# Optimization experiments

Hardware: AMD Instinct MI355X
Metric: run time of the kernel (lower is better)

The kernel has to match this reference:

```python
import jax, jax.numpy as jnp
import numpy as np

A = -0.75  # PyTorch bicubic convolution constant

def _cubic_weights(t):
    # t: fractional part in [0,1). Returns the 4 tap weights
    # (matches PyTorch get_cubic_upsample_coefficients with A=-0.75).
    t1 = t + 1.0
    w0 = ((A * t1 - 5.0 * A) * t1 + 8.0 * A) * t1 - 4.0 * A
    w1 = ((A + 2.0) * t - (A + 3.0)) * t * t + 1.0
    s = 1.0 - t
    w2 = ((A + 2.0) * s - (A + 3.0)) * s * s + 1.0
    s2 = 2.0 - t
    w3 = ((A * s2 - 5.0 * A) * s2 + 8.0 * A) * s2 - 4.0 * A
    return (w0, w1, w2, w3)

def _reflect_index(i, size):
    # integer reflection for padding_mode='reflection', align_corners=True over [0, size-1]
    span = size - 1
    if span <= 0:
        return jnp.zeros_like(i)
    m = jnp.abs(i) % (2 * span)
    return jnp.where(m > span, 2 * span - m, m)

def _bicubic_warp(x, flow):
    # x: [B,C,H,W], flow: [B,2,H,W] (flow[:,0]=dx, flow[:,1]=dy)
    B, C, H, W = x.shape
    gx = jnp.arange(W, dtype=x.dtype)
    gy = jnp.arange(H, dtype=x.dtype)
    # normalize-to-[-1,1] then grid_sample unnormalize (align_corners=True) cancel exactly:
    ix = gx[None, None, :] + flow[:, 0]  # [B,H,W] source x coord
    iy = gy[None, :, None] + flow[:, 1]  # [B,H,W] source y coord
    bx = jnp.floor(ix)
    by = jnp.floor(iy)
    tx = ix - bx
    ty = iy - by
    bx = bx.astype(jnp.int32)
    by = by.astype(jnp.int32)
    wx = _cubic_weights(tx)
    wy = _cubic_weights(ty)
    xf = x.reshape(B, C, H * W)
    out = jnp.zeros_like(x)
    for j in range(4):  # fixed 4x4 tap stencil
        Y = _reflect_index(by + (j - 1), H)
        for i in range(4):
            X = _reflect_index(bx + (i - 1), W)
            idx = (Y * W + X).reshape(B, 1, H * W)
            v = jnp.take_along_axis(xf, idx, axis=2).reshape(B, C, H, W)
            out = out + v * (wy[j] * wx[i])[:, None]
    return out

def setup_inputs() -> dict:
    key = jax.random.key(0)
    k1, k2, k3 = jax.random.split(key, 3)
    B, C, H, W = 8, 4, 1024, 1024
    return {
        "input": jax.random.normal(k1, (B, C, H, W), dtype=jnp.float32),
        "target": jax.random.normal(k2, (B, C, H, W), dtype=jnp.float32),
        "flow": jax.random.normal(k3, (B, 2, H, W), dtype=jnp.float32),
    }

def reference(input, target, flow):
    warped = _bicubic_warp(target, flow)
    b = 5
    return jnp.mean(jnp.abs(input[..., b:-b, b:-b] - warped[..., b:-b, b:-b]))
```

## Files before the change

kernel.cpp:

```cpp
#include <hip/hip_runtime.h>

constexpr int BB = 8, CC = 4, HH = 1024, WW = 1024, CROP = 5;
constexpr int HC = HH - 2 * CROP, WC = WW - 2 * CROP;
constexpr int HW = HH * WW;
constexpr float AA = -0.75f;

constexpr int NSTRIP = 16;
constexpr int GRID = 32 * NSTRIP * 2;
constexpr int RING = 16;
constexpr int SWID = 272;
constexpr int CH_STRIDE = RING * SWID;

typedef __attribute__((address_space(1))) const void gv_t;
typedef __attribute__((address_space(3))) void lv_t;

__device__ __forceinline__ int reflect_small(int i) {
    int r = i < 0 ? -i : i;
    return r > (HH - 1) ? 2 * (HH - 1) - r : r;
}

__device__ __forceinline__ void cubic_w(float t, float& w0, float& w1,
                                        float& w2, float& w3) {
    float t1 = t + 1.0f;
    w0 = ((AA * t1 - 5.0f * AA) * t1 + 8.0f * AA) * t1 - 4.0f * AA;
    w1 = ((AA + 2.0f) * t - (AA + 3.0f)) * t * t + 1.0f;
    float s = 1.0f - t;
    w2 = ((AA + 2.0f) * s - (AA + 3.0f)) * s * s + 1.0f;
    float s2 = 2.0f - t;
    w3 = ((AA * s2 - 5.0f * AA) * s2 + 8.0f * AA) * s2 - 4.0f * AA;
}

__device__ __noinline__ float px_slow2(const float* __restrict__ tgt_p,
                                       const float* __restrict__ in_p, int pix,
                                       int bx, int by, float wx0, float wx1,
                                       float wx2, float wx3, float wy0,
                                       float wy1, float wy2, float wy3) {
    const int r0 = reflect_small(by - 1) * WW;
    const int r1 = reflect_small(by) * WW;
    const int r2 = reflect_small(by + 1) * WW;
    const int r3 = reflect_small(by + 2) * WW;
    const int c0 = reflect_small(bx - 1);
    const int c1 = reflect_small(bx);
    const int c2 = reflect_small(bx + 1);
    const int c3 = reflect_small(bx + 2);
    float acc = 0.0f;
#pragma unroll
    for (int c = 0; c < 2; ++c) {
        const float* tb = tgt_p + c * HW;
        float q0 = wx0 * tb[r0 + c0] + wx1 * tb[r0 + c1] + wx2 * tb[r0 + c2] +
                   wx3 * tb[r0 + c3];
        float q1 = wx0 * tb[r1 + c0] + wx1 * tb[r1 + c1] + wx2 * tb[r1 + c2] +
                   wx3 * tb[r1 + c3];
        float q2 = wx0 * tb[r2 + c0] + wx1 * tb[r2 + c1] + wx2 * tb[r2 + c2] +
                   wx3 * tb[r2 + c3];
        float q3 = wx0 * tb[r3 + c0] + wx1 * tb[r3 + c1] + wx2 * tb[r3 + c2] +
                   wx3 * tb[r3 + c3];
        float v = wy0 * q0 + wy1 * q1 + wy2 * q2 + wy3 * q3;
        acc += fabsf(in_p[c * HW + pix] - v);
    }
    return acc;
}

__global__ __launch_bounds__(256, 4) void warp_loss_k(
    const float* __restrict__ input, const float* __restrict__ target,
    const float* __restrict__ flow, float* __restrict__ wsbuf) {
    __shared__ float cache[2 * CH_STRIDE];
    const int tid = (int)threadIdx.x;
    const int wv = tid >> 6, lane = tid & 63;

    const int low = (int)blockIdx.x & 511;
    const int pair = (int)blockIdx.x >> 9;
    const int colid = low >> 4;
    const int strip = low & 15;
    const int b = colid >> 2;
    const int chunk = colid & 3;
    const int x0 = CROP + chunk * 256;
    const int wscol = chunk == 0 ? 0 : chunk == 1 ? 252 : chunk == 2 ? 508 : 752;
    const int y0 = CROP + strip * 64;
    const int y1 = min(y0 + 64, CROP + HC);

    const int x = x0 + tid;
    const bool valid_px = x <= 1018;
    const int xc = valid_px ? x : 1018;

    const float* tgt_p = target + (size_t)b * CC * HW + (size_t)(pair * 2) * HW;
    const float* in_p = input + (size_t)b * CC * HW + (size_t)(pair * 2) * HW;
    const float* flow_b = flow + (size_t)b * 2 * HW;

    const int chv = wv >> 1, part = wv & 1;
    const float* plane = tgt_p + (size_t)chv * HW;
    const int chbase = chv * CH_STRIDE;

#pragma unroll 1
    for (int k = 0; k < 11; ++k) {
        const int r = y0 - 5 + k;
        const int slot = r & (RING - 1);
        const float* src = plane + (size_t)r * WW + wscol;
        if (part == 0) {
            __builtin_amdgcn_global_load_lds(
                (gv_t*)(src + lane * 4), (lv_t*)&cache[chbase + slot * SWID],
                16, 0, 0);
        } else {
            __builtin_amdgcn_global_load_lds(
                (gv_t*)(src + 208 + lane),
                (lv_t*)&cache[chbase + slot * SWID + 208], 4, 0, 0);
        }
    }
    __syncthreads();

    float lsum = 0.0f;

    for (int y = y0; y < y1; ++y) {
        {
            const int r = y + 6;
            if (r < HH) {
                const int slot = r & (RING - 1);
                const float* src = plane + (size_t)r * WW + wscol;
                if (part == 0) {
                    __builtin_amdgcn_global_load_lds(
                        (gv_t*)(src + lane * 4),
                        (lv_t*)&cache[chbase + slot * SWID], 16, 0, 0);
                } else {
                    __builtin_amdgcn_global_load_lds(
                        (gv_t*)(src + 208 + lane),
                        (lv_t*)&cache[chbase + slot * SWID + 208], 4, 0, 0);
                }
            }
        }

        const int pix = y * WW + xc;
        const float dx = flow_b[pix];
        const float dy = flow_b[HW + pix];
        const float i0v = in_p[pix];
        const float i1v = in_p[HW + pix];

        const float fx = (float)xc + dx;
        const float fy = (float)y + dy;
        const float bxf = floorf(fx), byf = floorf(fy);
        const int bx = (int)bxf, by = (int)byf;
        const float tx = fx - bxf, ty = fy - byf;

        float wx0, wx1, wx2, wx3, wy0, wy1, wy2, wy3;
        cubic_w(tx, wx0, wx1, wx2, wx3);
        cubic_w(ty, wy0, wy1, wy2, wy3);

        const int d = by - y;
        const int cx = bx - 1 - wscol;
        const bool fast =
            valid_px & (d >= -4) & (d <= 3) & (cx >= 0) & (cx <= 268);

        if (fast) {
            const int t = (by - 1) & (RING - 1);
            float v0 = 0.0f, v1 = 0.0f;
#pragma unroll
            for (int j = 0; j < 4; ++j) {
                const int s = (t + j) & (RING - 1);
                const int base = s * SWID + cx;
                const float wyj =
                    j == 0 ? wy0 : j == 1 ? wy1 : j == 2 ? wy2 : wy3;
                const float* p0 = &cache[base];
                const float* p1 = &cache[CH_STRIDE + base];
                v0 += wyj * (p0[0] * wx0 + p0[1] * wx1 + p0[2] * wx2 + p0[3] * wx3);
                v1 += wyj * (p1[0] * wx0 + p1[1] * wx1 + p1[2] * wx2 + p1[3] * wx3);
            }
            lsum += fabsf(i0v - v0) + fabsf(i1v - v1);
        } else if (valid_px) {
            lsum += px_slow2(tgt_p, in_p, pix, bx, by, wx0, wx1, wx2, wx3,
                             wy0, wy1, wy2, wy3);
        }

        __syncthreads();
    }

#pragma unroll
    for (int off2 = 32; off2 > 0; off2 >>= 1) lsum += __shfl_down(lsum, off2);

    __shared__ float sm[4];
    if (lane == 0) sm[wv] = lsum;
    __syncthreads();
    if (tid == 0) wsbuf[blockIdx.x] = sm[0] + sm[1] + sm[2] + sm[3];
}

__global__ __launch_bounds__(1024) void reduce_k(const float* __restrict__ ws,
                                                 float* __restrict__ out) {
    float s = 0.0f;
    for (int i = threadIdx.x; i < GRID; i += 1024) s += ws[i];
#pragma unroll
    for (int off = 32; off > 0; off >>= 1) s += __shfl_down(s, off);
    __shared__ float sm[16];
    const int lane = threadIdx.x & 63;
    const int wv = threadIdx.x >> 6;
    if (lane == 0) sm[wv] = s;
    __syncthreads();
    if (threadIdx.x == 0) {
        float t = 0.0f;
#pragma unroll
        for (int i = 0; i < 16; ++i) t += sm[i];
        constexpr float inv_count = 1.0f / ((float)BB * CC * HC * WC);
        out[0] = t * inv_count;
    }
}

extern "C" void kernel_launch(void* const* d_in, const int* in_sizes, int n_in,
                              void* d_out, int out_size, void* d_ws,
                              size_t ws_size, hipStream_t stream) {
    const float* input = (const float*)d_in[0];
    const float* target = (const float*)d_in[1];
    const float* flow = (const float*)d_in[2];
    float* ws = (float*)d_ws;
    float* out = (float*)d_out;

    warp_loss_k<<<GRID, 256, 0, stream>>>(input, target, flow, ws);
    reduce_k<<<1, 1024, 0, stream>>>(ws, out);
}
```

Baseline: 129.8 us.

## Interleave two channels in LDS cache and stage rows via registers

Replaces the direct global-to-LDS async loads with register-staged loads that interleave the two channels into float2 entries. The stencil then reads one 8-byte LDS word per tap for both channels, halving the LDS read instruction count. Global loads are issued before the compute so their latency overlaps it, and the LDS write happens after. The cost is extra VGPRs and VALU work for the staging, and only 34 of 64 lanes per wave do the loads.

Measured after the change: 136.6 us. 5.3% more time.

```diff
diff --git a/kernel.cpp b/kernel.cpp
--- a/kernel.cpp
+++ b/kernel.cpp
@@ -9,10 +9,9 @@
 constexpr int GRID = 32 * NSTRIP * 2;
 constexpr int RING = 16;
 constexpr int SWID = 272;
-constexpr int CH_STRIDE = RING * SWID;
-
-typedef __attribute__((address_space(1))) const void gv_t;
-typedef __attribute__((address_space(3))) void lv_t;
+
+typedef float f2 __attribute__((ext_vector_type(2)));
+typedef float f4 __attribute__((ext_vector_type(4)));
 
 __device__ __forceinline__ int reflect_small(int i) {
     int r = i < 0 ? -i : i;
@@ -64,7 +63,7 @@
 __global__ __launch_bounds__(256, 4) void warp_loss_k(
     const float* __restrict__ input, const float* __restrict__ target,
     const float* __restrict__ flow, float* __restrict__ wsbuf) {
-    __shared__ float cache[2 * CH_STRIDE];
+    __shared__ f2 cache2[RING * SWID];
     const int tid = (int)threadIdx.x;
     const int wv = tid >> 6, lane = tid & 63;
 
@@ -87,23 +86,19 @@
     const float* in_p = input + (size_t)b * CC * HW + (size_t)(pair * 2) * HW;
     const float* flow_b = flow + (size_t)b * 2 * HW;
 
-    const int chv = wv >> 1, part = wv & 1;
-    const float* plane = tgt_p + (size_t)chv * HW;
-    const int chbase = chv * CH_STRIDE;
+    const int c0 = wv * 68 + 2 * lane;
+    const bool stage_lane = lane < 34;
 
 #pragma unroll 1
     for (int k = 0; k < 11; ++k) {
         const int r = y0 - 5 + k;
-        const int slot = r & (RING - 1);
-        const float* src = plane + (size_t)r * WW + wscol;
-        if (part == 0) {
-            __builtin_amdgcn_global_load_lds(
-                (gv_t*)(src + lane * 4), (lv_t*)&cache[chbase + slot * SWID],
-                16, 0, 0);
-        } else {
-            __builtin_amdgcn_global_load_lds(
-                (gv_t*)(src + 208 + lane),
-                (lv_t*)&cache[chbase + slot * SWID + 208], 4, 0, 0);
+        if (stage_lane) {
+            const float* s0 = tgt_p + (size_t)r * WW + wscol + c0;
+            f2 g0 = *(const f2*)s0;
+            f2 g1 = *(const f2*)(s0 + HW);
+            f4 val;
+            val.x = g0.x; val.y = g1.x; val.z = g0.y; val.w = g1.y;
+            *(f4*)&cache2[(r & (RING - 1)) * SWID + c0] = val;
         }
     }
     __syncthreads();
@@ -111,21 +106,13 @@
     float lsum = 0.0f;
 
     for (int y = y0; y < y1; ++y) {
-        {
-            const int r = y + 6;
-            if (r < HH) {
-                const int slot = r & (RING - 1);
-                const float* src = plane + (size_t)r * WW + wscol;
-                if (part == 0) {
-                    __builtin_amdgcn_global_load_lds(
-                        (gv_t*)(src + lane * 4),
-                        (lv_t*)&cache[chbase + slot * SWID], 16, 0, 0);
-                } else {
-                    __builtin_amdgcn_global_load_lds(
-                        (gv_t*)(src + 208 + lane),
-                        (lv_t*)&cache[chbase + slot * SWID + 208], 4, 0, 0);
-                }
-            }
+        const int r = y + 6;
+        const bool do_stage = (r < HH) & stage_lane;
+        f2 g0 = {0.0f, 0.0f}, g1 = {0.0f, 0.0f};
+        if (do_stage) {
+            const float* s0 = tgt_p + (size_t)r * WW + wscol + c0;
+            g0 = *(const f2*)s0;
+            g1 = *(const f2*)(s0 + HW);
         }
 
         const int pix = y * WW + xc;
@@ -155,18 +142,23 @@
 #pragma unroll
             for (int j = 0; j < 4; ++j) {
                 const int s = (t + j) & (RING - 1);
-                const int base = s * SWID + cx;
+                const f2* p = &cache2[s * SWID + cx];
+                f2 a0 = p[0], a1 = p[1], a2 = p[2], a3 = p[3];
                 const float wyj =
                     j == 0 ? wy0 : j == 1 ? wy1 : j == 2 ? wy2 : wy3;
-                const float* p0 = &cache[base];
-                const float* p1 = &cache[CH_STRIDE + base];
-                v0 += wyj * (p0[0] * wx0 + p0[1] * wx1 + p0[2] * wx2 + p0[3] * wx3);
-                v1 += wyj * (p1[0] * wx0 + p1[1] * wx1 + p1[2] * wx2 + p1[3] * wx3);
+                v0 += wyj * (a0.x * wx0 + a1.x * wx1 + a2.x * wx2 + a3.x * wx3);
+                v1 += wyj * (a0.y * wx0 + a1.y * wx1 + a2.y * wx2 + a3.y * wx3);
             }
             lsum += fabsf(i0v - v0) + fabsf(i1v - v1);
         } else if (valid_px) {
             lsum += px_slow2(tgt_p, in_p, pix, bx, by, wx0, wx1, wx2, wx3,
                              wy0, wy1, wy2, wy3);
+        }
+
+        if (do_stage) {
+            f4 val;
+            val.x = g0.x; val.y = g1.x; val.z = g0.y; val.w = g1.y;
+            *(f4*)&cache2[(r & (RING - 1)) * SWID + c0] = val;
         }
 
         __syncthreads();
```

## Process two rows per iteration and prefetch flow/input one step ahead

Applied to the files above, without the earlier changes.

The main loop now handles two output rows per iteration. It fetches the next pair's flow and input values into registers one iteration early and streams two LDS ring rows per iteration, with one extra row preloaded. This is meant to hide global load latency behind the stencil math and halve the number of block-wide barriers. The fast-path row windows are widened per sub-row to match the deeper ring lookahead. The cost is more register pressure and a row-pair assumption that relies on each strip having an even number of rows.

After: 109.2 us (median of 2 runs). -15.9%, faster.

```diff
diff --git a/kernel.cpp b/kernel.cpp
--- a/kernel.cpp
+++ b/kernel.cpp
@@ -92,7 +92,7 @@
     const int chbase = chv * CH_STRIDE;
 
 #pragma unroll 1
-    for (int k = 0; k < 11; ++k) {
+    for (int k = 0; k < 12; ++k) {
         const int r = y0 - 5 + k;
         const int slot = r & (RING - 1);
         const float* src = plane + (size_t)r * WW + wscol;
@@ -106,13 +106,46 @@
                 (lv_t*)&cache[chbase + slot * SWID + 208], 4, 0, 0);
         }
     }
+
+    float dx0n, dy0n, i00n, i01n, dx1n, dy1n, i10n, i11n;
+    {
+        const int p0 = y0 * WW + xc;
+        const int p1 = (y0 + 1) * WW + xc;
+        dx0n = flow_b[p0];
+        dy0n = flow_b[HW + p0];
+        i00n = in_p[p0];
+        i01n = in_p[HW + p0];
+        dx1n = flow_b[p1];
+        dy1n = flow_b[HW + p1];
+        i10n = in_p[p1];
+        i11n = in_p[HW + p1];
+    }
+
     __syncthreads();
 
     float lsum = 0.0f;
 
-    for (int y = y0; y < y1; ++y) {
+    for (int y = y0; y < y1; y += 2) {
+        const float dx0 = dx0n, dy0 = dy0n, i00 = i00n, i01 = i01n;
+        const float dx1 = dx1n, dy1 = dy1n, i10 = i10n, i11 = i11n;
+
         {
-            const int r = y + 6;
+            const int yn = (y + 2 < y1) ? y + 2 : y;
+            const int p0 = yn * WW + xc;
+            const int p1 = (yn + 1) * WW + xc;
+            dx0n = flow_b[p0];
+            dy0n = flow_b[HW + p0];
+            i00n = in_p[p0];
+            i01n = in_p[HW + p0];
+            dx1n = flow_b[p1];
+            dy1n = flow_b[HW + p1];
+            i10n = in_p[p1];
+            i11n = in_p[HW + p1];
+        }
+
+#pragma unroll
+        for (int rr = 0; rr < 2; ++rr) {
+            const int r = y + 7 + rr;
             if (r < HH) {
                 const int slot = r & (RING - 1);
                 const float* src = plane + (size_t)r * WW + wscol;
@@ -128,45 +161,85 @@
             }
         }
 
-        const int pix = y * WW + xc;
-        const float dx = flow_b[pix];
-        const float dy = flow_b[HW + pix];
-        const float i0v = in_p[pix];
-        const float i1v = in_p[HW + pix];
-
-        const float fx = (float)xc + dx;
-        const float fy = (float)y + dy;
-        const float bxf = floorf(fx), byf = floorf(fy);
-        const int bx = (int)bxf, by = (int)byf;
-        const float tx = fx - bxf, ty = fy - byf;
-
-        float wx0, wx1, wx2, wx3, wy0, wy1, wy2, wy3;
-        cubic_w(tx, wx0, wx1, wx2, wx3);
-        cubic_w(ty, wy0, wy1, wy2, wy3);
-
-        const int d = by - y;
-        const int cx = bx - 1 - wscol;
-        const bool fast =
-            valid_px & (d >= -4) & (d <= 3) & (cx >= 0) & (cx <= 268);
-
-        if (fast) {
-            const int t = (by - 1) & (RING - 1);
-            float v0 = 0.0f, v1 = 0.0f;
-#pragma unroll
-            for (int j = 0; j < 4; ++j) {
-                const int s = (t + j) & (RING - 1);
-                const int base = s * SWID + cx;
-                const float wyj =
-                    j == 0 ? wy0 : j == 1 ? wy1 : j == 2 ? wy2 : wy3;
-                const float* p0 = &cache[base];
-                const float* p1 = &cache[CH_STRIDE + base];
-                v0 += wyj * (p0[0] * wx0 + p0[1] * wx1 + p0[2] * wx2 + p0[3] * wx3);
-                v1 += wyj * (p1[0] * wx0 + p1[1] * wx1 + p1[2] * wx2 + p1[3] * wx3);
+        {
+            const int pix = y * WW + xc;
+            const float fx = (float)xc + dx0;
+            const float fy = (float)y + dy0;
+            const float bxf = floorf(fx), byf = floorf(fy);
+            const int bx = (int)bxf, by = (int)byf;
+            const float tx = fx - bxf, ty = fy - byf;
+
+            float wx0, wx1, wx2, wx3, wy0, wy1, wy2, wy3;
+            cubic_w(tx, wx0, wx1, wx2, wx3);
+            cubic_w(ty, wy0, wy1, wy2, wy3);
+
+            const int d = by - y;
+            const int cx = bx - 1 - wscol;
+            const bool fast =
+                valid_px & (d >= -4) & (d <= 4) & (cx >= 0) & (cx <= 268);
+
+            if (fast) {
+                const int t = (by - 1) & (RING - 1);
+                float v0 = 0.0f, v1 = 0.0f;
+#pragma unroll
+                for (int j = 0; j < 4; ++j) {
+                    const int s = (t + j) & (RING - 1);
+                    const int base = s * SWID + cx;
+                    const float wyj =
+                        j == 0 ? wy0 : j == 1 ? wy1 : j == 2 ? wy2 : wy3;
+                    const float* p0 = &cache[base];
+                    const float* p1 = &cache[CH_STRIDE + base];
+                    v0 += wyj * (p0[0] * wx0 + p0[1] * wx1 + p0[2] * wx2 +
+                                 p0[3] * wx3);
+                    v1 += wyj * (p1[0] * wx0 + p1[1] * wx1 + p1[2] * wx2 +
+                                 p1[3] * wx3);
+                }
+                lsum += fabsf(i00 - v0) + fabsf(i01 - v1);
+            } else if (valid_px) {
+                lsum += px_slow2(tgt_p, in_p, pix, bx, by, wx0, wx1, wx2, wx3,
+                                 wy0, wy1, wy2, wy3);
             }
-            lsum += fabsf(i0v - v0) + fabsf(i1v - v1);
-        } else if (valid_px) {
-            lsum += px_slow2(tgt_p, in_p, pix, bx, by, wx0, wx1, wx2, wx3,
-                             wy0, wy1, wy2, wy3);
+        }
+
+        {
+            const int yb = y + 1;
+            const int pix = yb * WW + xc;
+            const float fx = (float)xc + dx1;
+            const float fy = (float)yb + dy1;
+            const float bxf = floorf(fx), byf = floorf(fy);
+            const int bx = (int)bxf, by = (int)byf;
+            const float tx = fx - bxf, ty = fy - byf;
+
+            float wx0, wx1, wx2, wx3, wy0, wy1, wy2, wy3;
+            cubic_w(tx, wx0, wx1, wx2, wx3);
+            cubic_w(ty, wy0, wy1, wy2, wy3);
+
+            const int d = by - yb;
+            const int cx = bx - 1 - wscol;
+            const bool fast =
+                valid_px & (d >= -5) & (d <= 3) & (cx >= 0) & (cx <= 268);
+
+            if (fast) {
+                const int t = (by - 1) & (RING - 1);
+                float v0 = 0.0f, v1 = 0.0f;
+#pragma unroll
+                for (int j = 0; j < 4; ++j) {
+                    const int s = (t + j) & (RING - 1);
+                    const int base = s * SWID + cx;
+                    const float wyj =
+                        j == 0 ? wy0 : j == 1 ? wy1 : j == 2 ? wy2 : wy3;
+                    const float* p0 = &cache[base];
+                    const float* p1 = &cache[CH_STRIDE + base];
+                    v0 += wyj * (p0[0] * wx0 + p0[1] * wx1 + p0[2] * wx2 +
+                                 p0[3] * wx3);
+                    v1 += wyj * (p1[0] * wx0 + p1[1] * wx1 + p1[2] * wx2 +
+                                 p1[3] * wx3);
+                }
+                lsum += fabsf(i10 - v0) + fabsf(i11 - v1);
+            } else if (valid_px) {
+                lsum += px_slow2(tgt_p, in_p, pix, bx, by, wx0, wx1, wx2, wx3,
+                                 wy0, wy1, wy2, wy3);
+            }
         }
 
         __syncthreads();
```
